# Optimization experiments

Hardware: AMD Instinct MI355X
Metric: run time of the kernel (lower is better)

## Reference

```python
import jax, jax.numpy as jnp
import numpy as np

B, C, H, W, K = 4, 64, 128, 128, 3
K2 = K * K
PAD = (K - 1) // 2  # same padding for 3x3


def setup_inputs() -> dict:
    key = jax.random.key(0)
    ks = jax.random.split(key, 9)
    s = 0.05
    return {
        "x": jax.random.normal(ks[0], (B, C, H, W), jnp.float32),
        "inter": jax.random.normal(ks[1], (B, C, H, W), jnp.float32),
        # offset/mask predictor conv: input cat([x, inter]) -> 3*K2 channels (dy, dx, mask)
        "w_offset": jax.random.normal(ks[2], (3 * K2, 2 * C, K, K), jnp.float32) * s,
        "b_offset": jnp.zeros((3 * K2,), jnp.float32),
        # deformable conv weight (bias=False per DGM init)
        "w_dcn": jax.random.normal(ks[3], (C, C, K, K), jnp.float32) * s,
        # SFT gamma branch: two 1x1 convs (bias=False)
        "w_g1": jax.random.normal(ks[4], (C, C), jnp.float32) * s,
        "w_g2": jax.random.normal(ks[5], (C, C), jnp.float32) * s,
        # SFT beta branch: two 1x1 convs (bias=False)
        "w_b1": jax.random.normal(ks[6], (C, C), jnp.float32) * s,
        "w_b2": jax.random.normal(ks[7], (C, C), jnp.float32) * s,
    }


def _lrelu(v):
    # LeakyReLU(0.1)
    return jnp.where(v >= 0, v, 0.1 * v)


def _conv(x, w, b=None):
    y = jax.lax.conv_general_dilated(
        x, w, window_strides=(1, 1), padding=[(PAD, PAD), (PAD, PAD)],
        dimension_numbers=("NCHW", "OIHW", "NCHW"))
    if b is not None:
        y = y + b[None, :, None, None]
    return y


def _bilinear_gather(x, py, px):
    """x: [B,C,H,W]; py, px: [B,K2,H,W] float sample coords.
    Returns samples [B,K2,H,W,C]; out-of-bounds treated as zero (DCN zero-pad)."""
    y0 = jnp.floor(py)
    x0 = jnp.floor(px)
    wy = (py - y0)[..., None]
    wx = (px - x0)[..., None]

    def gather(yi, xi):
        valid = ((yi >= 0) & (yi < H) & (xi >= 0) & (xi < W)).astype(x.dtype)
        yc = jnp.clip(yi, 0, H - 1).astype(jnp.int32)
        xc = jnp.clip(xi, 0, W - 1).astype(jnp.int32)
        bidx = jnp.arange(B)[:, None, None, None]
        v = x[bidx, :, yc, xc]  # advanced indexing -> [B,K2,H,W,C]
        return v * valid[..., None]

    v00 = gather(y0, x0)
    v01 = gather(y0, x0 + 1)
    v10 = gather(y0 + 1, x0)
    v11 = gather(y0 + 1, x0 + 1)
    return (v00 * (1 - wy) * (1 - wx) + v01 * (1 - wy) * wx
            + v10 * wy * (1 - wx) + v11 * wy * wx)


def _dgm_forward(x, inter, w_offset, b_offset, w_dcn, w_g1, w_g2, w_b1, w_b2):
    # --- WADCN branch: modulated deformable conv, offsets predicted from cat(x, inter)
    om = _conv(jnp.concatenate([x, inter], axis=1), w_offset, b_offset)  # [B,3K2,H,W]
    dy, dx, m = jnp.split(om, 3, axis=1)  # each [B,K2,H,W]
    mask = jax.nn.sigmoid(m)

    ky, kx = jnp.meshgrid(jnp.arange(K), jnp.arange(K), indexing="ij")
    ky = ky.reshape(K2).astype(x.dtype)
    kx = kx.reshape(K2).astype(x.dtype)
    hh = jnp.arange(H, dtype=x.dtype)
    ww = jnp.arange(W, dtype=x.dtype)
    # sample coords: base grid + kernel-tap offset + learned offset
    py = hh[None, None, :, None] + (ky - PAD)[None, :, None, None] + dy  # [B,K2,H,W]
    px = ww[None, None, None, :] + (kx - PAD)[None, :, None, None] + dx

    samp = _bilinear_gather(x, py, px) * mask[..., None]  # [B,K2,H,W,C]
    dcn_out = jnp.einsum("bkhwc,ock->bohw", samp, w_dcn.reshape(C, C, K2))

    # --- SFT branch: two 1x1-conv + LeakyReLU chains producing gamma/beta
    gamma = jnp.einsum("oc,bchw->bohw", w_g2,
                       _lrelu(jnp.einsum("oc,bchw->bohw", w_g1, inter)))
    beta = jnp.einsum("oc,bchw->bohw", w_b2,
                      _lrelu(jnp.einsum("oc,bchw->bohw", w_b1, inter)))
    sft_out = x * gamma + beta

    # --- fused residual combine (DGM.relu is defined but never applied)
    return x + dcn_out + sft_out


def reference(x, inter, w_offset, b_offset, w_dcn, w_g1, w_g2, w_b1, w_b2):
    return _dgm_forward(x, inter, w_offset, b_offset, w_dcn, w_g1, w_g2, w_b1, w_b2)
```

## Files before the change

### kernel.cpp

```cpp
#include <hip/hip_runtime.h>
#include <hip/hip_bf16.h>
#include <math.h>

#define BB 4
#define CC 64
#define HH 128
#define WW 128
#define HW (HH*WW)
#define NPIX (BB*HW)

typedef __attribute__((ext_vector_type(8))) short short8;
typedef __attribute__((ext_vector_type(4))) float f32x4;

__device__ __forceinline__ float bf2f(ushort u) {
  union { unsigned u; float f; } v; v.u = ((unsigned)u) << 16; return v.f;
}
__device__ __forceinline__ ushort f2bf(float f) {
  __hip_bfloat16 h = __float2bfloat16(f); return *(ushort*)&h;
}

__global__ __launch_bounds__(256) void k_prep(
    const float* __restrict__ x, const float* __restrict__ inter,
    const float* __restrict__ w_off, const float* __restrict__ w_dcn,
    const float* __restrict__ wg1, const float* __restrict__ wb1,
    const float* __restrict__ wg2, const float* __restrict__ wb2,
    ushort* __restrict__ x_clh, ushort* __restrict__ inter_clh,
    ushort* __restrict__ wfb, ushort* __restrict__ wdT,
    ushort* __restrict__ w1gb, ushort* __restrict__ w1bb,
    ushort* __restrict__ w2gb, ushort* __restrict__ w2bb,
    float* __restrict__ zp) {
  __shared__ __align__(16) float tile[64 * 128];
  int blk = blockIdx.x;
  int tid = threadIdx.x;
  if (blk < 1024) {
    int sel = blk >> 9;
    int bh = blk & 511;
    int b = bh >> 7, h = bh & 127;
    const float* src = sel ? inter : x;
    ushort* dst = sel ? inter_clh : x_clh;
    const float* sp = src + (size_t)(b * 64) * HW + h * WW;
#pragma unroll
    for (int it = 0; it < 8; ++it) {
      int idx = it * 256 + tid;
      int c = idx >> 5, wq = idx & 31;
      float4 v = *(const float4*)(sp + (size_t)c * HW + wq * 4);
      int s = (c >> 3) & 7;
      *(float4*)(&tile[c * 128 + ((wq ^ s) << 2)]) = v;
    }
    __syncthreads();
    ushort* dp = dst + ((size_t)b * HW + h * WW) * 64;
#pragma unroll
    for (int it = 0; it < 4; ++it) {
      int idx = it * 256 + tid;
      int w = idx >> 3, c8 = idx & 7;
      short8 outv;
#pragma unroll
      for (int j = 0; j < 8; ++j) {
        int c = c8 * 8 + j;
        int sl = (w >> 2) ^ c8;
        float f = tile[c * 128 + (sl << 2) + (w & 3)];
        outv[j] = (short)f2bf(f);
      }
      *(short8*)(dp + (size_t)w * 64 + c8 * 8) = outv;
    }
  } else if (blk < 1168) {
    int i = (blk - 1024) * 256 + tid;
    if (i < 64) zp[i] = 0.f;
    if (i < 9 * 32 * 128) {
      int tap = i >> 12, rem = i & 4095, m = rem >> 7, c = rem & 127;
      float v = (m < 27) ? w_off[(size_t)(m * 128 + c) * 9 + tap] : 0.f;
      wfb[i] = f2bf(v);
    }
  } else if (blk < 1312) {
    int i = (blk - 1168) * 256 + tid;
    if (i < 64 * 64 * 9) {
      int o = i / 576, rem = i % 576, k = rem >> 6, c = rem & 63;
      wdT[i] = f2bf(w_dcn[(o * 64 + c) * 9 + k]);
    }
  } else {
    int i = (blk - 1312) * 256 + tid;
    int m = i >> 12, j = i & 4095;
    const float* src = (m == 0) ? wg1 : (m == 1) ? wb1 : (m == 2) ? wg2 : wb2;
    ushort* dst = (m == 0) ? w1gb : (m == 1) ? w1bb : (m == 2) ? w2gb : w2bb;
    dst[j] = f2bf(src[j]);
  }
}

#define CPITCH 72
#define SPITCH 200
#define NPX 32
#define FPX 72

__global__ __launch_bounds__(256) void k_omega(
    const float* __restrict__ x, const ushort* __restrict__ x_clh,
    const ushort* __restrict__ inter_clh,
    const float* __restrict__ b_off, const ushort* __restrict__ wfb,
    const ushort* __restrict__ wdT,
    const ushort* __restrict__ w1gb, const ushort* __restrict__ w1bb,
    const ushort* __restrict__ w2gb, const ushort* __restrict__ w2bb,
    const ushort* __restrict__ zp16, float* __restrict__ out) {
  __shared__ __align__(16) ushort LDSB[9280];
  ushort* halo = LDSB;
  ushort* Sg = LDSB;
  ushort* Sb = LDSB + 2304;
  float* oml = (float*)(LDSB + 4608);
  int*   cy  = (int*)LDSB;
  int*   cx  = cy + 288;
  float* cwy = (float*)(cx + 288);
  float* cwx = cwy + 288;
  float* cm  = cwx + 288;
  ushort* S  = LDSB + 2880;

  int tid = threadIdx.x;
  int wave = tid >> 6, lane = tid & 63;
  int quad = lane >> 4, col = lane & 15;
  int rr = lane >> 3, g = lane & 7;
  int bid = blockIdx.x;
  int wid = (bid & 7) * 256 + (bid >> 3);
  int pg0 = wid * NPX;
  int b = pg0 >> 14, hw0 = pg0 & 16383;
  int h = hw0 >> 7, w0 = hw0 & 127;
  int pt = wave >> 1, mt = wave & 1;
  int o_base = __builtin_amdgcn_readfirstlane(wave * 16);

  f32x4 accx = {0.f, 0.f, 0.f, 0.f}, acci = {0.f, 0.f, 0.f, 0.f};
  {
    int ch = (tid & 7) * 8;
    unsigned bbase = (unsigned)b * HW;
    const ushort* wb0 = wfb + (size_t)(mt * 16 + col) * 128 + quad * 8;
    int pxb = pt * 16 + col;
#pragma unroll 1
    for (int pass = 0; pass < 2; ++pass) {
      const ushort* sb = pass ? inter_clh : x_clh;
#pragma unroll
      for (int it = 0; it < 4; ++it) {
        int e = it * 32 + (tid >> 3);
        if (e < 102) {
          int row = e / 34, pxl = e % 34;
          int hs = h + row - 1;
          int ps = w0 + pxl - 1;
          bool ok = ((unsigned)hs < 128u) && ((unsigned)ps < 128u);
          int hc = hs < 0 ? 0 : (hs > 127 ? 127 : hs);
          int pc = ps < 0 ? 0 : (ps > 127 ? 127 : ps);
          short8 v = *(const short8*)(sb + ((size_t)(bbase + (hc << 7) + pc)) * 64 + ch);
          short8 z = {0, 0, 0, 0, 0, 0, 0, 0};
          if (!ok) v = z;
          *(short8*)(&halo[e * CPITCH + ch]) = v;
        }
      }
      __syncthreads();
      int aoff = pass ? 64 : 0;
      f32x4 accp = {0.f, 0.f, 0.f, 0.f};
#pragma unroll
      for (int ky = 0; ky < 3; ++ky) {
#pragma unroll
        for (int kx = 0; kx < 3; ++kx) {
          int tap = ky * 3 + kx;
          const ushort* wt = wb0 + (size_t)tap * 4096 + aoff;
#pragma unroll
          for (int ks = 0; ks < 2; ++ks) {
            short8 a0 = *(const short8*)(wt + ks * 32);
            short8 b0 = *(const short8*)(&halo[(ky * 34 + pxb + kx) * CPITCH + ks * 32 + quad * 8]);
            accp = __builtin_amdgcn_mfma_f32_16x16x32_bf16(a0, b0, accp, 0, 0, 0);
          }
        }
      }
      if (pass) acci = accp; else accx = accp;
      __syncthreads();
    }
  }

#pragma unroll
  for (int r = 0; r < 4; ++r) {
    int o = mt * 16 + quad * 4 + r;
    if (o < 27) oml[o * 33 + pt * 16 + col] = accx[r] + acci[r];
  }

  f32x4 ag[2], ab[2];
#pragma unroll
  for (int nt = 0; nt < 2; ++nt) {
    ag[nt] = (f32x4){0.f, 0.f, 0.f, 0.f};
    ab[nt] = (f32x4){0.f, 0.f, 0.f, 0.f};
  }
#pragma unroll
  for (int ks = 0; ks < 2; ++ks) {
    short8 a_g = *(const short8*)(w1gb + (size_t)(o_base + col) * 64 + ks * 32 + quad * 8);
    short8 a_b = *(const short8*)(w1bb + (size_t)(o_base + col) * 64 + ks * 32 + quad * 8);
#pragma unroll
    for (int nt = 0; nt < 2; ++nt) {
      short8 bf = *(const short8*)(inter_clh + (size_t)(pg0 + nt * 16 + col) * 64 + ks * 32 + quad * 8);
      ag[nt] = __builtin_amdgcn_mfma_f32_16x16x32_bf16(a_g, bf, ag[nt], 0, 0, 0);
      ab[nt] = __builtin_amdgcn_mfma_f32_16x16x32_bf16(a_b, bf, ab[nt], 0, 0, 0);
    }
  }
#pragma unroll
  for (int nt = 0; nt < 2; ++nt) {
    int px = nt * 16 + col;
    ushort pkg[4], pkb[4];
#pragma unroll
    for (int r = 0; r < 4; ++r) {
      float vg = ag[nt][r]; vg = vg >= 0.f ? vg : 0.1f * vg;
      float vb = ab[nt][r]; vb = vb >= 0.f ? vb : 0.1f * vb;
      pkg[r] = f2bf(vg); pkb[r] = f2bf(vb);
    }
    *(uint2*)(&Sg[px * FPX + o_base + quad * 4]) = *(uint2*)pkg;
    *(uint2*)(&Sb[px * FPX + o_base + quad * 4]) = *(uint2*)pkb;
  }
  __syncthreads();

  f32x4 gg[2], gb[2];
#pragma unroll
  for (int nt = 0; nt < 2; ++nt) {
    gg[nt] = (f32x4){0.f, 0.f, 0.f, 0.f};
    gb[nt] = (f32x4){0.f, 0.f, 0.f, 0.f};
  }
#pragma unroll
  for (int ks = 0; ks < 2; ++ks) {
    short8 a_g = *(const short8*)(w2gb + (size_t)(o_base + col) * 64 + ks * 32 + quad * 8);
    short8 a_b = *(const short8*)(w2bb + (size_t)(o_base + col) * 64 + ks * 32 + quad * 8);
#pragma unroll
    for (int nt = 0; nt < 2; ++nt) {
      short8 bgf = *(const short8*)(Sg + (nt * 16 + col) * FPX + ks * 32 + quad * 8);
      short8 bbf = *(const short8*)(Sb + (nt * 16 + col) * FPX + ks * 32 + quad * 8);
      gg[nt] = __builtin_amdgcn_mfma_f32_16x16x32_bf16(a_g, bgf, gg[nt], 0, 0, 0);
      gb[nt] = __builtin_amdgcn_mfma_f32_16x16x32_bf16(a_b, bbf, gb[nt], 0, 0, 0);
    }
  }
  float xv[2][4];
#pragma unroll
  for (int nt = 0; nt < 2; ++nt)
#pragma unroll
    for (int r = 0; r < 4; ++r) {
      int o = o_base + quad * 4 + r;
      xv[nt][r] = x[(size_t)(b * 64 + o) * HW + hw0 + nt * 16 + col];
    }
  __syncthreads();

  for (int i = tid; i < 9 * NPX; i += 256) {
    int k = i >> 5, p = i & 31;
    float dy = oml[k * 33 + p] + b_off[k];
    float dx = oml[(9 + k) * 33 + p] + b_off[9 + k];
    float mz = oml[(18 + k) * 33 + p] + b_off[18 + k];
    float py = (float)(h + (k / 3) - 1) + dy;
    float px = (float)(w0 + p + (k % 3) - 1) + dx;
    float y0f = floorf(py), x0f = floorf(px);
    cy[i] = (int)y0f;
    cx[i] = (int)x0f;
    cwy[i] = py - y0f;
    cwx[i] = px - x0f;
    cm[i] = 1.f / (1.f + __expf(-mz));
  }

  f32x4 acc[2];
  acc[0] = (f32x4){0.f, 0.f, 0.f, 0.f};
  acc[1] = (f32x4){0.f, 0.f, 0.f, 0.f};

  const ushort* bp = x_clh + (size_t)b * HW * 64;

  for (int chunk = 0; chunk < 3; ++chunk) {
    __syncthreads();
#pragma unroll
    for (int it = 0; it < 3; ++it) {
      int p = wave * 8 + rr;
      int idx = (chunk * 3 + it) * NPX + p;
      int y0 = cy[idx], x0 = cx[idx];
      float wy = cwy[idx], wx = cwx[idx], m = cm[idx];
      bool yok0 = (unsigned)y0 < 128u, yok1 = (unsigned)(y0 + 1) < 128u;
      bool xok0 = (unsigned)x0 < 128u, xok1 = (unsigned)(x0 + 1) < 128u;
      const ushort* r0 = bp + ((size_t)(int)((y0 << 7) + x0)) * 64 + g * 8;
      const ushort* r1 = r0 + (size_t)WW * 64;
      short8 s00 = *(const short8*)((yok0 && xok0) ? r0 : zp16);
      short8 s01 = *(const short8*)((yok0 && xok1) ? (r0 + 64) : zp16);
      short8 s10 = *(const short8*)((yok1 && xok0) ? r1 : zp16);
      short8 s11 = *(const short8*)((yok1 && xok1) ? (r1 + 64) : zp16);
      short8 outv;
#pragma unroll
      for (int j = 0; j < 8; ++j) {
        float v00 = bf2f((ushort)s00[j]), v01 = bf2f((ushort)s01[j]);
        float v10 = bf2f((ushort)s10[j]), v11 = bf2f((ushort)s11[j]);
        float top = v00 + (v01 - v00) * wx;
        float bot = v10 + (v11 - v10) * wx;
        float val = top + (bot - top) * wy;
        outv[j] = (short)f2bf(val * m);
      }
      *(short8*)(&S[p * SPITCH + it * 64 + g * 8]) = outv;
    }
    __syncthreads();
    const ushort* wrow = wdT + (size_t)(o_base + col) * 576 + chunk * 192 + quad * 8;
    const ushort* srow = S + quad * 8;
#pragma unroll
    for (int ks = 0; ks < 6; ++ks) {
      short8 a = *(const short8*)(wrow + ks * 32);
#pragma unroll
      for (int nt = 0; nt < 2; ++nt) {
        short8 bf = *(const short8*)(srow + (nt * 16 + col) * SPITCH + ks * 32);
        acc[nt] = __builtin_amdgcn_mfma_f32_16x16x32_bf16(a, bf, acc[nt], 0, 0, 0);
      }
    }
  }

#pragma unroll
  for (int nt = 0; nt < 2; ++nt) {
#pragma unroll
    for (int r = 0; r < 4; ++r) {
      int o = o_base + quad * 4 + r;
      size_t idx = (size_t)(b * 64 + o) * HW + hw0 + nt * 16 + col;
      out[idx] = xv[nt][r] + xv[nt][r] * gg[nt][r] + gb[nt][r] + acc[nt][r];
    }
  }
}

extern "C" void kernel_launch(void* const* d_in, const int* in_sizes, int n_in,
                              void* d_out, int out_size, void* d_ws, size_t ws_size,
                              hipStream_t stream) {
  const float* x     = (const float*)d_in[0];
  const float* inter = (const float*)d_in[1];
  const float* w_off = (const float*)d_in[2];
  const float* b_off = (const float*)d_in[3];
  const float* w_dcn = (const float*)d_in[4];
  const float* wg1   = (const float*)d_in[5];
  const float* wg2   = (const float*)d_in[6];
  const float* wb1   = (const float*)d_in[7];
  const float* wb2   = (const float*)d_in[8];
  float* out = (float*)d_out;

  float* ws        = (float*)d_ws;
  ushort* x_clh    = (ushort*)ws;
  ushort* inter_clh= (ushort*)(ws + 2097152);
  ushort* wfb      = (ushort*)(ws + 4194304);
  ushort* wdT      = (ushort*)(ws + 4212736);
  ushort* w1gb     = (ushort*)(ws + 4231168);
  ushort* w1bb     = (ushort*)(ws + 4233216);
  ushort* w2gb     = (ushort*)(ws + 4235264);
  ushort* w2bb     = (ushort*)(ws + 4237312);
  float* zp        = ws + 4239360;

  k_prep<<<1376, 256, 0, stream>>>(x, inter, w_off, w_dcn, wg1, wb1, wg2, wb2,
                                   x_clh, inter_clh, wfb, wdT,
                                   w1gb, w1bb, w2gb, w2bb, zp);

  k_omega<<<2048, 256, 0, stream>>>(x, x_clh, inter_clh, b_off, wfb, wdT,
                                    w1gb, w1bb, w2gb, w2bb,
                                    (const ushort*)zp, out);
}
```

Measured before the change: 172.3 us.

## Double pixels per block to 64 and restructure DCN gather into two halves

Each block now handles 64 pixels instead of 32, so the offset-conv halo (3 rows of 66 pixels) and the weight fragments are reused across twice as many outputs, and the grid drops to 1024 blocks. The deformable gather is reorganized so all 9 taps for 32 pixels are staged in shared memory at once, and one 18-step MFMA pass runs per half instead of three chunked passes. This cuts halo overfetch and barrier count per pixel. The cost is about 48KB of shared memory and more accumulator registers per block, which can lower occupancy and latency hiding in the gather.

```diff
diff --git a/kernel.cpp b/kernel.cpp
--- a/kernel.cpp
+++ b/kernel.cpp
@@ -86,10 +86,9 @@
   }
 }
 
-#define CPITCH 72
-#define SPITCH 200
-#define NPX 32
+#define NPX 64
 #define FPX 72
+#define SP2 584
 
 __global__ __launch_bounds__(256) void k_omega(
     const float* __restrict__ x, const ushort* __restrict__ x_clh,
@@ -99,44 +98,43 @@
     const ushort* __restrict__ w1gb, const ushort* __restrict__ w1bb,
     const ushort* __restrict__ w2gb, const ushort* __restrict__ w2bb,
     const ushort* __restrict__ zp16, float* __restrict__ out) {
-  __shared__ __align__(16) ushort LDSB[9280];
+  __shared__ __align__(16) ushort LDSB[24448];
   ushort* halo = LDSB;
   ushort* Sg = LDSB;
-  ushort* Sb = LDSB + 2304;
-  float* oml = (float*)(LDSB + 4608);
+  ushort* Sb = LDSB + 4608;
+  float* oml = (float*)(LDSB + 9216);
   int*   cy  = (int*)LDSB;
-  int*   cx  = cy + 288;
-  float* cwy = (float*)(cx + 288);
-  float* cwx = cwy + 288;
-  float* cm  = cwx + 288;
-  ushort* S  = LDSB + 2880;
+  int*   cx  = cy + 576;
+  float* cwy = (float*)(cx + 576);
+  float* cwx = cwy + 576;
+  float* cm  = cwx + 576;
+  ushort* S  = LDSB + 5760;
 
   int tid = threadIdx.x;
   int wave = tid >> 6, lane = tid & 63;
   int quad = lane >> 4, col = lane & 15;
-  int rr = lane >> 3, g = lane & 7;
+  int g = tid & 7;
   int bid = blockIdx.x;
-  int wid = (bid & 7) * 256 + (bid >> 3);
+  int wid = (bid & 7) * 128 + (bid >> 3);
   int pg0 = wid * NPX;
   int b = pg0 >> 14, hw0 = pg0 & 16383;
   int h = hw0 >> 7, w0 = hw0 & 127;
   int pt = wave >> 1, mt = wave & 1;
   int o_base = __builtin_amdgcn_readfirstlane(wave * 16);
 
-  f32x4 accx = {0.f, 0.f, 0.f, 0.f}, acci = {0.f, 0.f, 0.f, 0.f};
+  f32x4 accx[2], acci[2];
   {
     int ch = (tid & 7) * 8;
     unsigned bbase = (unsigned)b * HW;
     const ushort* wb0 = wfb + (size_t)(mt * 16 + col) * 128 + quad * 8;
-    int pxb = pt * 16 + col;
 #pragma unroll 1
     for (int pass = 0; pass < 2; ++pass) {
       const ushort* sb = pass ? inter_clh : x_clh;
 #pragma unroll
-      for (int it = 0; it < 4; ++it) {
+      for (int it = 0; it < 7; ++it) {
         int e = it * 32 + (tid >> 3);
-        if (e < 102) {
-          int row = e / 34, pxl = e % 34;
+        if (e < 198) {
+          int row = e / 66, pxl = e % 66;
           int hs = h + row - 1;
           int ps = w0 + pxl - 1;
           bool ok = ((unsigned)hs < 128u) && ((unsigned)ps < 128u);
@@ -145,40 +143,44 @@
           short8 v = *(const short8*)(sb + ((size_t)(bbase + (hc << 7) + pc)) * 64 + ch);
           short8 z = {0, 0, 0, 0, 0, 0, 0, 0};
           if (!ok) v = z;
-          *(short8*)(&halo[e * CPITCH + ch]) = v;
+          *(short8*)(&halo[e * 72 + ch]) = v;
         }
       }
       __syncthreads();
       int aoff = pass ? 64 : 0;
-      f32x4 accp = {0.f, 0.f, 0.f, 0.f};
+      f32x4 ap0 = {0.f, 0.f, 0.f, 0.f}, ap1 = {0.f, 0.f, 0.f, 0.f};
 #pragma unroll
       for (int ky = 0; ky < 3; ++ky) {
 #pragma unroll
         for (int kx = 0; kx < 3; ++kx) {
-          int tap = ky * 3 + kx;
-          const ushort* wt = wb0 + (size_t)tap * 4096 + aoff;
+          const ushort* wt = wb0 + (size_t)(ky * 3 + kx) * 4096 + aoff;
 #pragma unroll
           for (int ks = 0; ks < 2; ++ks) {
-            short8 a0 = *(const short8*)(wt + ks * 32);
-            short8 b0 = *(const short8*)(&halo[(ky * 34 + pxb + kx) * CPITCH + ks * 32 + quad * 8]);
-            accp = __builtin_amdgcn_mfma_f32_16x16x32_bf16(a0, b0, accp, 0, 0, 0);
+            short8 a = *(const short8*)(wt + ks * 32);
+            short8 b0 = *(const short8*)(&halo[(ky * 66 + pt * 32 + col + kx) * 72 + ks * 32 + quad * 8]);
+            ap0 = __builtin_amdgcn_mfma_f32_16x16x32_bf16(a, b0, ap0, 0, 0, 0);
+            short8 b1 = *(const short8*)(&halo[(ky * 66 + pt * 32 + 16 + col + kx) * 72 + ks * 32 + quad * 8]);
+            ap1 = __builtin_amdgcn_mfma_f32_16x16x32_bf16(a, b1, ap1, 0, 0, 0);
           }
         }
       }
-      if (pass) acci = accp; else accx = accp;
+      if (pass) { acci[0] = ap0; acci[1] = ap1; }
+      else      { accx[0] = ap0; accx[1] = ap1; }
       __syncthreads();
     }
   }
 
 #pragma unroll
-  for (int r = 0; r < 4; ++r) {
-    int o = mt * 16 + quad * 4 + r;
-    if (o < 27) oml[o * 33 + pt * 16 + col] = accx[r] + acci[r];
-  }
-
-  f32x4 ag[2], ab[2];
-#pragma unroll
-  for (int nt = 0; nt < 2; ++nt) {
+  for (int nt2 = 0; nt2 < 2; ++nt2)
+#pragma unroll
+    for (int r = 0; r < 4; ++r) {
+      int o = mt * 16 + quad * 4 + r;
+      if (o < 27) oml[o * 66 + pt * 32 + nt2 * 16 + col] = accx[nt2][r] + acci[nt2][r];
+    }
+
+  f32x4 ag[4], ab[4];
+#pragma unroll
+  for (int nt = 0; nt < 4; ++nt) {
     ag[nt] = (f32x4){0.f, 0.f, 0.f, 0.f};
     ab[nt] = (f32x4){0.f, 0.f, 0.f, 0.f};
   }
@@ -187,14 +189,14 @@
     short8 a_g = *(const short8*)(w1gb + (size_t)(o_base + col) * 64 + ks * 32 + quad * 8);
     short8 a_b = *(const short8*)(w1bb + (size_t)(o_base + col) * 64 + ks * 32 + quad * 8);
 #pragma unroll
-    for (int nt = 0; nt < 2; ++nt) {
+    for (int nt = 0; nt < 4; ++nt) {
       short8 bf = *(const short8*)(inter_clh + (size_t)(pg0 + nt * 16 + col) * 64 + ks * 32 + quad * 8);
       ag[nt] = __builtin_amdgcn_mfma_f32_16x16x32_bf16(a_g, bf, ag[nt], 0, 0, 0);
       ab[nt] = __builtin_amdgcn_mfma_f32_16x16x32_bf16(a_b, bf, ab[nt], 0, 0, 0);
     }
   }
 #pragma unroll
-  for (int nt = 0; nt < 2; ++nt) {
+  for (int nt = 0; nt < 4; ++nt) {
     int px = nt * 16 + col;
     ushort pkg[4], pkb[4];
 #pragma unroll
@@ -208,9 +210,9 @@
   }
   __syncthreads();
 
-  f32x4 gg[2], gb[2];
-#pragma unroll
-  for (int nt = 0; nt < 2; ++nt) {
+  f32x4 gg[4], gb[4];
+#pragma unroll
+  for (int nt = 0; nt < 4; ++nt) {
     gg[nt] = (f32x4){0.f, 0.f, 0.f, 0.f};
     gb[nt] = (f32x4){0.f, 0.f, 0.f, 0.f};
   }
@@ -219,30 +221,31 @@
     short8 a_g = *(const short8*)(w2gb + (size_t)(o_base + col) * 64 + ks * 32 + quad * 8);
     short8 a_b = *(const short8*)(w2bb + (size_t)(o_base + col) * 64 + ks * 32 + quad * 8);
 #pragma unroll
-    for (int nt = 0; nt < 2; ++nt) {
+    for (int nt = 0; nt < 4; ++nt) {
       short8 bgf = *(const short8*)(Sg + (nt * 16 + col) * FPX + ks * 32 + quad * 8);
       short8 bbf = *(const short8*)(Sb + (nt * 16 + col) * FPX + ks * 32 + quad * 8);
       gg[nt] = __builtin_amdgcn_mfma_f32_16x16x32_bf16(a_g, bgf, gg[nt], 0, 0, 0);
       gb[nt] = __builtin_amdgcn_mfma_f32_16x16x32_bf16(a_b, bbf, gb[nt], 0, 0, 0);
     }
   }
-  float xv[2][4];
-#pragma unroll
-  for (int nt = 0; nt < 2; ++nt)
+  float ev[4][4];
+#pragma unroll
+  for (int nt = 0; nt < 4; ++nt)
 #pragma unroll
     for (int r = 0; r < 4; ++r) {
       int o = o_base + quad * 4 + r;
-      xv[nt][r] = x[(size_t)(b * 64 + o) * HW + hw0 + nt * 16 + col];
+      float xv = x[(size_t)(b * 64 + o) * HW + hw0 + nt * 16 + col];
+      ev[nt][r] = xv + xv * gg[nt][r] + gb[nt][r];
     }
   __syncthreads();
 
   for (int i = tid; i < 9 * NPX; i += 256) {
-    int k = i >> 5, p = i & 31;
-    float dy = oml[k * 33 + p] + b_off[k];
-    float dx = oml[(9 + k) * 33 + p] + b_off[9 + k];
-    float mz = oml[(18 + k) * 33 + p] + b_off[18 + k];
-    float py = (float)(h + (k / 3) - 1) + dy;
-    float px = (float)(w0 + p + (k % 3) - 1) + dx;
+    int t = i >> 6, p = i & 63;
+    float dy = oml[t * 66 + p] + b_off[t];
+    float dx = oml[(9 + t) * 66 + p] + b_off[9 + t];
+    float mz = oml[(18 + t) * 66 + p] + b_off[18 + t];
+    float py = (float)(h + (t / 3) - 1) + dy;
+    float px = (float)(w0 + p + (t % 3) - 1) + dx;
     float y0f = floorf(py), x0f = floorf(px);
     cy[i] = (int)y0f;
     cx[i] = (int)x0f;
@@ -250,19 +253,21 @@
     cwx[i] = px - x0f;
     cm[i] = 1.f / (1.f + __expf(-mz));
   }
-
-  f32x4 acc[2];
-  acc[0] = (f32x4){0.f, 0.f, 0.f, 0.f};
-  acc[1] = (f32x4){0.f, 0.f, 0.f, 0.f};
+  __syncthreads();
+
+  f32x4 acc[4];
+#pragma unroll
+  for (int nt = 0; nt < 4; ++nt) acc[nt] = (f32x4){0.f, 0.f, 0.f, 0.f};
 
   const ushort* bp = x_clh + (size_t)b * HW * 64;
-
-  for (int chunk = 0; chunk < 3; ++chunk) {
-    __syncthreads();
-#pragma unroll
-    for (int it = 0; it < 3; ++it) {
-      int p = wave * 8 + rr;
-      int idx = (chunk * 3 + it) * NPX + p;
+  int p = tid >> 3;
+
+#pragma unroll 1
+  for (int half = 0; half < 2; ++half) {
+    if (half) __syncthreads();
+#pragma unroll 3
+    for (int t = 0; t < 9; ++t) {
+      int idx = t * 64 + half * 32 + p;
       int y0 = cy[idx], x0 = cx[idx];
       float wy = cwy[idx], wx = cwx[idx], m = cm[idx];
       bool yok0 = (unsigned)y0 < 128u, yok1 = (unsigned)(y0 + 1) < 128u;
@@ -283,31 +288,30 @@
         float val = top + (bot - top) * wy;
         outv[j] = (short)f2bf(val * m);
       }
-      *(short8*)(&S[p * SPITCH + it * 64 + g * 8]) = outv;
+      *(short8*)(&S[p * SP2 + t * 64 + g * 8]) = outv;
     }
     __syncthreads();
-    const ushort* wrow = wdT + (size_t)(o_base + col) * 576 + chunk * 192 + quad * 8;
+    const ushort* wrow = wdT + (size_t)(o_base + col) * 576 + quad * 8;
     const ushort* srow = S + quad * 8;
 #pragma unroll
-    for (int ks = 0; ks < 6; ++ks) {
+    for (int ks = 0; ks < 18; ++ks) {
       short8 a = *(const short8*)(wrow + ks * 32);
 #pragma unroll
-      for (int nt = 0; nt < 2; ++nt) {
-        short8 bf = *(const short8*)(srow + (nt * 16 + col) * SPITCH + ks * 32);
-        acc[nt] = __builtin_amdgcn_mfma_f32_16x16x32_bf16(a, bf, acc[nt], 0, 0, 0);
-      }
-    }
-  }
-
-#pragma unroll
-  for (int nt = 0; nt < 2; ++nt) {
+      for (int ntl = 0; ntl < 2; ++ntl) {
+        short8 bfv = *(const short8*)(srow + (ntl * 16 + col) * SP2 + ks * 32);
+        acc[half * 2 + ntl] = __builtin_amdgcn_mfma_f32_16x16x32_bf16(a, bfv, acc[half * 2 + ntl], 0, 0, 0);
+      }
+    }
+  }
+
+#pragma unroll
+  for (int nt = 0; nt < 4; ++nt)
 #pragma unroll
     for (int r = 0; r < 4; ++r) {
       int o = o_base + quad * 4 + r;
       size_t idx = (size_t)(b * 64 + o) * HW + hw0 + nt * 16 + col;
-      out[idx] = xv[nt][r] + xv[nt][r] * gg[nt][r] + gb[nt][r] + acc[nt][r];
-    }
-  }
+      out[idx] = ev[nt][r] + acc[nt][r];
+    }
 }
 
 extern "C" void kernel_launch(void* const* d_in, const int* in_sizes, int n_in,
@@ -339,7 +343,7 @@
                                    x_clh, inter_clh, wfb, wdT,
                                    w1gb, w1bb, w2gb, w2bb, zp);
 
-  k_omega<<<2048, 256, 0, stream>>>(x, x_clh, inter_clh, b_off, wfb, wdT,
+  k_omega<<<1024, 256, 0, stream>>>(x, x_clh, inter_clh, b_off, wfb, wdT,
                                     w1gb, w1bb, w2gb, w2bb,
                                     (const ushort*)zp, out);
 }
```

New measurement: 166.9 us. -3.1%, faster.
